# Optimization experiments

Hardware: AMD Instinct MI355X
Metric: run time of the kernel (lower is better)

The kernel has to match this reference:

```python
import math
import jax, jax.numpy as jnp
import numpy as np
from jax import lax

B = 4; N = 4096; F = 15; A = 24          # batch, tcr_num, feature_num, aa_num
HID = 10; H = 1; HD = 10; AFN = 14       # attn hidden, heads, head dim, sum(filter_num)
KS = [2, 3, 4, 5, 6, 7]; FN = [3, 3, 3, 2, 2, 1]
K = int(N * 0.05)                        # routing topk = 204
SCALE = np.float32(1.0 / math.sqrt(HD))


def setup_inputs() -> dict:
    key = jax.random.key(0)
    ks = jax.random.split(key, 24)
    inp = {"x": jax.random.normal(ks[0], (B, N, F, A), jnp.float32)}
    for i, (h, f) in enumerate(zip(KS, FN)):
        inp["conv_w%d" % h] = jax.random.normal(ks[1 + 2 * i], (f, F, h), jnp.float32) * 0.1
        inp["conv_b%d" % h] = jax.random.normal(ks[2 + 2 * i], (f,), jnp.float32) * 0.1
    specs = [("q", HID, AFN), ("k", HID, AFN), ("v", HID, AFN), ("attn", AFN, HID), ("mil", 2, AFN)]
    for j, (nm, o, i_) in enumerate(specs):
        inp["w_" + nm] = jax.random.normal(ks[13 + 2 * j], (o, i_), jnp.float32) * 0.1
        inp["b_" + nm] = jax.random.normal(ks[14 + 2 * j], (o,), jnp.float32) * 0.1
    return inp


def reference(x, conv_w2, conv_b2, conv_w3, conv_b3, conv_w4, conv_b4,
              conv_w5, conv_b5, conv_w6, conv_b6, conv_w7, conv_b7,
              w_q, b_q, w_k, b_k, w_v, b_v, w_attn, b_attn, w_mil, b_mil):
    # --- per-sequence conv feature extraction ---
    xc = x.reshape(-1, F, A)  # [B*N, 15, 24]
    feats = []
    for w, b in [(conv_w2, conv_b2), (conv_w3, conv_b3), (conv_w4, conv_b4),
                 (conv_w5, conv_b5), (conv_w6, conv_b6), (conv_w7, conv_b7)]:
        y = lax.conv_general_dilated(xc, w, (1,), 'VALID',
                                     dimension_numbers=('NCH', 'OIH', 'NCH'))
        y = jax.nn.relu(y + b[None, :, None])
        feats.append(jnp.max(y, axis=-1))  # AdaptiveMaxPool1d(1)
    out = jnp.concatenate(feats, axis=1).reshape(B, N, AFN)  # [B, N, 14]

    # --- QKV projections, split into heads -> [B, H, N, HD] ---
    q = (out @ w_q.T + b_q).reshape(B, N, H, HD).transpose(0, 2, 1, 3)
    k = (out @ w_k.T + b_k).reshape(B, N, H, HD).transpose(0, 2, 1, 3)
    v = (out @ w_v.T + b_v).reshape(B, N, H, HD).transpose(0, 2, 1, 3)

    # --- bi-level routing: full scores, topk over head-mean (detached in torch) ---
    scores_raw = jnp.einsum('bhnd,bhmd->bhnm', q, k)  # [B, H, N, N]
    a_r = jnp.mean(lax.stop_gradient(scores_raw), axis=1)  # [B, N, N]
    _, idx = lax.top_k(a_r, K)  # [B, N, K] int32
    idx_r = jnp.broadcast_to(idx[:, None], (B, H, N, K))

    scores = jnp.take_along_axis(scores_raw * SCALE, idx_r, axis=3)  # [B, H, N, K]
    # gather values per (batch, head, query): v_g[b,h,i,j] = v[b,h,idx[b,h,i,j]]
    v_g = jax.vmap(jax.vmap(lambda vh, ih: vh[ih]))(v, idx_r)  # [B, H, N, K, HD]

    probs = jax.nn.softmax(scores, axis=-1)  # dropout is identity at p=0 / eval
    ctx = jnp.einsum('bhnk,bhnkd->bhnd', probs, v_g)  # [B, H, N, HD]
    ctx = ctx.transpose(0, 2, 1, 3).reshape(B, N, HID)

    ctx = ctx @ w_attn.T + b_attn          # [B, N, 14]
    logits = ctx @ w_mil.T + b_mil          # [B, N, 2]
    pooled = jnp.sum(logits, axis=1) / N    # [B, 2]
    return pooled, probs[:, :, :, None, :]  # probs shaped [B, H, N, 1, K] as in torch
```

## Files before the change

### kernel.cpp

```cpp
#include <hip/hip_runtime.h>
#include <math.h>

#define NB 4
#define NN 4096
#define KSEL 204
#define NBINS 512
#define CANDN 256
#define QKSCALE 0.31622776601683794f

#define WS_Q 0
#define WS_KT (NB * NN * 10)
#define WS_V (2 * NB * NN * 10)
#define WS_LG (3 * NB * NN * 10)

#define SEQ_PER_BLOCK 16

__global__ __launch_bounds__(256) void featqkv_kernel(
    const float* __restrict__ x,
    const float* __restrict__ w2, const float* __restrict__ b2,
    const float* __restrict__ w3, const float* __restrict__ b3,
    const float* __restrict__ w4, const float* __restrict__ b4,
    const float* __restrict__ w5, const float* __restrict__ b5,
    const float* __restrict__ w6, const float* __restrict__ b6,
    const float* __restrict__ w7, const float* __restrict__ b7,
    const float* __restrict__ wq, const float* __restrict__ bq,
    const float* __restrict__ wk, const float* __restrict__ bk,
    const float* __restrict__ wv, const float* __restrict__ bv,
    float* __restrict__ q_out, float* __restrict__ kT_out, float* __restrict__ v_out)
{
    __shared__ float xs[SEQ_PER_BLOCK * 360];
    __shared__ float wconv[840];
    __shared__ float bconv[14];
    __shared__ float wqkv[420];
    __shared__ float bqkv[30];
    __shared__ float feats[SEQ_PER_BLOCK * 14];

    const int t = threadIdx.x;
    const int g0 = blockIdx.x * SEQ_PER_BLOCK;

    const float* xg = x + (size_t)g0 * 360;
    for (int i = t; i < SEQ_PER_BLOCK * 360; i += 256) xs[i] = xg[i];
    for (int i = t; i < 90; i += 256) wconv[i] = w2[i];
    for (int i = t; i < 135; i += 256) wconv[90 + i] = w3[i];
    for (int i = t; i < 180; i += 256) wconv[225 + i] = w4[i];
    for (int i = t; i < 150; i += 256) wconv[405 + i] = w5[i];
    for (int i = t; i < 180; i += 256) wconv[555 + i] = w6[i];
    for (int i = t; i < 105; i += 256) wconv[735 + i] = w7[i];
    if (t < 3) bconv[t] = b2[t];
    else if (t < 6) bconv[t] = b3[t - 3];
    else if (t < 9) bconv[t] = b4[t - 6];
    else if (t < 11) bconv[t] = b5[t - 9];
    else if (t < 13) bconv[t] = b6[t - 11];
    else if (t == 13) bconv[t] = b7[0];
    for (int i = t; i < 140; i += 256) wqkv[i] = wq[i];
    for (int i = t; i < 140; i += 256) wqkv[140 + i] = wk[i];
    for (int i = t; i < 140; i += 256) wqkv[280 + i] = wv[i];
    if (t < 10) bqkv[t] = bq[t];
    else if (t < 20) bqkv[t] = bk[t - 10];
    else if (t < 30) bqkv[t] = bv[t - 20];
    __syncthreads();

    const int seq = t >> 4;
    const int wkr = t & 15;

    if (wkr < 14) {
        const int ch = wkr;
        int h, fi, woff;
        if (ch < 3)       { h = 2; fi = ch;      woff = 0   + fi * 30; }
        else if (ch < 6)  { h = 3; fi = ch - 3;  woff = 90  + fi * 45; }
        else if (ch < 9)  { h = 4; fi = ch - 6;  woff = 225 + fi * 60; }
        else if (ch < 11) { h = 5; fi = ch - 9;  woff = 405 + fi * 75; }
        else if (ch < 13) { h = 6; fi = ch - 11; woff = 555 + fi * 90; }
        else              { h = 7; fi = 0;       woff = 735; }
        const int T = 24 - h + 1;

        float acc[23];
#pragma unroll
        for (int i2 = 0; i2 < 23; i2++) acc[i2] = 0.f;
        const float* xrow = &xs[seq * 360];
        for (int c = 0; c < 15; c++) {
            float xr[24];
#pragma unroll
            for (int u = 0; u < 24; u++) xr[u] = xrow[c * 24 + u];
#pragma unroll
            for (int j = 0; j < 7; j++) {
                if (j < h) {
                    float wv_ = wconv[woff + c * h + j];
#pragma unroll
                    for (int tt = 0; tt < 23; tt++) {
                        if (tt < T) acc[tt] = fmaf(xr[tt + j], wv_, acc[tt]);
                    }
                }
            }
        }
        float m = -1e30f;
#pragma unroll
        for (int tt = 0; tt < 23; tt++) {
            if (tt < T) m = fmaxf(m, acc[tt]);
        }
        feats[seq * 14 + ch] = fmaxf(m + bconv[ch], 0.f);
    }
    __syncthreads();

    const int g = g0 + seq;
    const int b_ = g >> 12;
    const int n_ = g & 4095;
    for (int o = wkr; o < 30; o += 16) {
        const int type = o / 10;
        const int comp = o % 10;
        const float* wrow = &wqkv[type * 140 + comp * 14];
        const float* frow = &feats[seq * 14];
        float a = bqkv[type * 10 + comp];
#pragma unroll
        for (int ii = 0; ii < 14; ii++) a = fmaf(frow[ii], wrow[ii], a);
        if (type == 0) q_out[(size_t)g * 10 + comp] = a;
        else if (type == 1) kT_out[((size_t)b_ * 10 + comp) * NN + n_] = a;
        else v_out[(size_t)g * 10 + comp] = a;
    }
}

__device__ __forceinline__ float dec_key(unsigned int k) {
    return (k & 0x80000000u) ? __uint_as_float(k ^ 0x80000000u)
                             : __uint_as_float(~k);
}
__device__ __forceinline__ unsigned int enc_key(float s) {
    unsigned int u = __float_as_uint(s);
    return (u & 0x80000000u) ? ~u : (u | 0x80000000u);
}

__global__ __launch_bounds__(256, 6) void attn_kernel(
    const float* __restrict__ qbuf, const float* __restrict__ kTbuf,
    const float* __restrict__ vbuf,
    const float* __restrict__ w_attn, const float* __restrict__ b_attn,
    const float* __restrict__ w_mil, const float* __restrict__ b_mil,
    float* __restrict__ out_probs, float* __restrict__ logits)
{
    __shared__ unsigned int base_[NBINS];
    __shared__ unsigned int bc_[NBINS];
    __shared__ unsigned long long cand[CANDN];
    __shared__ float hpart[4], lpart[4], fpart[4];
    __shared__ unsigned int wtot[4];
    __shared__ float ctxp[40];
    __shared__ float ctx_sh[10];
    __shared__ float attn_sh[14];

    const int t = threadIdx.x;
    const int lane = t & 63;
    const int w = t >> 6;
    const int row = blockIdx.x;
    const int b_ = row >> 12;

    float q0, q1, q2, q3, q4, q5, q6, q7, q8, q9;
    {
        const float* qp = qbuf + (size_t)row * 10;
        q0 = qp[0]; q1 = qp[1]; q2 = qp[2]; q3 = qp[3]; q4 = qp[4];
        q5 = qp[5]; q6 = qp[6]; q7 = qp[7]; q8 = qp[8]; q9 = qp[9];
    }
    const float* kTb = kTbuf + (size_t)b_ * 10 * NN;
    float sc[16];
    float vhi = -1e30f, vlo = 1e30f;
#pragma unroll
    for (int i = 0; i < 4; i++) {
        float4 a0 = make_float4(0.f, 0.f, 0.f, 0.f);
#pragma unroll
        for (int c = 0; c < 10; c++) {
            const float qc = (c == 0) ? q0 : (c == 1) ? q1 : (c == 2) ? q2 : (c == 3) ? q3 :
                             (c == 4) ? q4 : (c == 5) ? q5 : (c == 6) ? q6 : (c == 7) ? q7 :
                             (c == 8) ? q8 : q9;
            const float4 kv = reinterpret_cast<const float4*>(kTb + c * NN)[i * 256 + t];
            a0.x = fmaf(qc, kv.x, a0.x);
            a0.y = fmaf(qc, kv.y, a0.y);
            a0.z = fmaf(qc, kv.z, a0.z);
            a0.w = fmaf(qc, kv.w, a0.w);
        }
        sc[i * 4 + 0] = a0.x; sc[i * 4 + 1] = a0.y;
        sc[i * 4 + 2] = a0.z; sc[i * 4 + 3] = a0.w;
        vhi = fmaxf(vhi, fmaxf(fmaxf(a0.x, a0.y), fmaxf(a0.z, a0.w)));
        vlo = fminf(vlo, fminf(fminf(a0.x, a0.y), fminf(a0.z, a0.w)));
    }
#pragma unroll
    for (int off = 32; off > 0; off >>= 1) {
        vhi = fmaxf(vhi, __shfl_xor(vhi, off));
        vlo = fminf(vlo, __shfl_xor(vlo, off));
    }
    if (lane == 0) { hpart[w] = vhi; lpart[w] = vlo; }
    base_[2 * t] = 0u; base_[2 * t + 1] = 0u;
    cand[t] = 0ULL;
    __syncthreads();
    const float hi = fmaxf(fmaxf(hpart[0], hpart[1]), fmaxf(hpart[2], hpart[3]));
    const float lo = fminf(fminf(lpart[0], lpart[1]), fminf(lpart[2], lpart[3]));
    const bool degen = (hi <= lo);

    float pv = 0.f;
    int jj = 0, p = KSEL;
    bool selected = false;
    const float smax = hi * QKSCALE;

    if (!degen) {
        const float scale = (float)(NBINS - 1) / (hi - lo);

#pragma unroll
        for (int i = 0; i < 16; i++) {
            const int bin = (int)fminf((sc[i] - lo) * scale, (float)(NBINS - 1));
            atomicAdd(&base_[bin], 1u);
        }
        __syncthreads();

        {
            const unsigned int c0 = base_[2 * t];
            const unsigned int c1 = base_[2 * t + 1];
            const unsigned int T_ = c0 + c1;
            unsigned int acc = T_;
#pragma unroll
            for (int off = 1; off < 64; off <<= 1) {
                unsigned int o = __shfl_down(acc, off);
                if (lane + off < 64) acc += o;
            }
            if (lane == 0) wtot[w] = acc;
            __syncthreads();
            unsigned int tail = 0u;
#pragma unroll
            for (int w2 = 1; w2 < 4; w2++) if (w2 > w) tail += wtot[w2];
            const unsigned int A = (acc - T_) + tail;
            base_[2 * t + 1] = A;
            base_[2 * t] = A + c1;
            bc_[2 * t + 1] = A;
            bc_[2 * t] = A + c1;
        }
        __syncthreads();

#pragma unroll
        for (int i = 0; i < 16; i++) {
            const int bin = (int)fminf((sc[i] - lo) * scale, (float)(NBINS - 1));
            const unsigned int bs = base_[bin];
            if (bs < KSEL) {
                const unsigned int pos = atomicAdd(&bc_[bin], 1u);
                if (pos < CANDN) {
                    const int j = (i >> 2) * 1024 + t * 4 + (i & 3);
                    cand[pos] = (((unsigned long long)enc_key(sc[i])) << 16)
                              | (unsigned long long)(4095 - j);
                }
            }
        }
        __syncthreads();

        const unsigned long long mine = cand[t];
        if (mine != 0ULL) {
            const float s = dec_key((unsigned int)(mine >> 16));
            const int bin = (int)fminf((s - lo) * scale, (float)(NBINS - 1));
            const unsigned int bs = base_[bin];
            unsigned int end = (bin < NBINS - 1) ? 0u : 0u;
            end = (bin == NBINS - 1) ? bs + (4096u) : base_[bin + 1];
            unsigned int e2 = (bin > 0) ? base_[bin - 1] : 4096u;
            if (e2 > CANDN) e2 = CANDN;
            unsigned int rank = 0;
            for (unsigned int s2 = bs; s2 < e2; s2++)
                rank += (cand[s2] > mine) ? 1u : 0u;
            const unsigned int pp = bs + rank;
            if (pp < KSEL) {
                selected = true;
                p = (int)pp;
                jj = 4095 - (int)(mine & 0xFFFFu);
                pv = expf(s * QKSCALE - smax);
            }
        }
    } else {
        if (t < KSEL) {
            selected = true;
            p = t;
            jj = t;
            pv = 1.f;
        }
    }

    float dsum = pv;
#pragma unroll
    for (int off = 32; off > 0; off >>= 1) dsum += __shfl_xor(dsum, off);
    if (lane == 0) fpart[w] = dsum;
    __syncthreads();
    const float inv = 1.f / (fpart[0] + fpart[1] + fpart[2] + fpart[3]);

    float cx0 = 0.f, cx1 = 0.f, cx2 = 0.f, cx3 = 0.f, cx4 = 0.f;
    float cx5 = 0.f, cx6 = 0.f, cx7 = 0.f, cx8 = 0.f, cx9 = 0.f;
    if (selected) {
        const float pn = pv * inv;
        out_probs[(size_t)row * KSEL + p] = pn;
        const float* vr = vbuf + ((size_t)b_ * NN + (size_t)jj) * 10;
        const float2 v01 = reinterpret_cast<const float2*>(vr)[0];
        const float2 v23 = reinterpret_cast<const float2*>(vr)[1];
        const float2 v45 = reinterpret_cast<const float2*>(vr)[2];
        const float2 v67 = reinterpret_cast<const float2*>(vr)[3];
        const float2 v89 = reinterpret_cast<const float2*>(vr)[4];
        cx0 = pn * v01.x; cx1 = pn * v01.y;
        cx2 = pn * v23.x; cx3 = pn * v23.y;
        cx4 = pn * v45.x; cx5 = pn * v45.y;
        cx6 = pn * v67.x; cx7 = pn * v67.y;
        cx8 = pn * v89.x; cx9 = pn * v89.y;
    }
#pragma unroll
    for (int off = 32; off > 0; off >>= 1) {
        cx0 += __shfl_xor(cx0, off); cx1 += __shfl_xor(cx1, off);
        cx2 += __shfl_xor(cx2, off); cx3 += __shfl_xor(cx3, off);
        cx4 += __shfl_xor(cx4, off); cx5 += __shfl_xor(cx5, off);
        cx6 += __shfl_xor(cx6, off); cx7 += __shfl_xor(cx7, off);
        cx8 += __shfl_xor(cx8, off); cx9 += __shfl_xor(cx9, off);
    }
    if (lane == 0) {
        ctxp[w * 10 + 0] = cx0; ctxp[w * 10 + 1] = cx1; ctxp[w * 10 + 2] = cx2;
        ctxp[w * 10 + 3] = cx3; ctxp[w * 10 + 4] = cx4; ctxp[w * 10 + 5] = cx5;
        ctxp[w * 10 + 6] = cx6; ctxp[w * 10 + 7] = cx7; ctxp[w * 10 + 8] = cx8;
        ctxp[w * 10 + 9] = cx9;
    }
    __syncthreads();
    if (t < 10) ctx_sh[t] = ctxp[t] + ctxp[10 + t] + ctxp[20 + t] + ctxp[30 + t];
    __syncthreads();

    if (t < 14) {
        float a = b_attn[t];
#pragma unroll
        for (int d = 0; d < 10; d++) a = fmaf(ctx_sh[d], w_attn[t * 10 + d], a);
        attn_sh[t] = a;
    }
    __syncthreads();
    if (t < 2) {
        float lg = b_mil[t];
#pragma unroll
        for (int ii = 0; ii < 14; ii++) lg = fmaf(attn_sh[ii], w_mil[t * 14 + ii], lg);
        logits[(size_t)row * 2 + t] = lg;
    }
}

__global__ __launch_bounds__(256) void pool_kernel(
    const float* __restrict__ logits, float* __restrict__ out)
{
    __shared__ float red[256];
    const int t = threadIdx.x;
    const int bc = blockIdx.x;
    const int b_ = bc >> 1;
    const int c_ = bc & 1;
    float a = 0.f;
    for (int n2 = t; n2 < NN; n2 += 256)
        a += logits[((size_t)b_ * NN + n2) * 2 + c_];
    red[t] = a;
    __syncthreads();
    for (int off = 128; off > 0; off >>= 1) {
        if (t < off) red[t] += red[t + off];
        __syncthreads();
    }
    if (t == 0) out[bc] = red[0] * (1.f / 4096.f);
}

extern "C" void kernel_launch(void* const* d_in, const int* in_sizes, int n_in,
                              void* d_out, int out_size, void* d_ws, size_t ws_size,
                              hipStream_t stream) {
    const float* x  = (const float*)d_in[0];
    const float* w2 = (const float*)d_in[1];  const float* b2 = (const float*)d_in[2];
    const float* w3 = (const float*)d_in[3];  const float* b3 = (const float*)d_in[4];
    const float* w4 = (const float*)d_in[5];  const float* b4 = (const float*)d_in[6];
    const float* w5 = (const float*)d_in[7];  const float* b5 = (const float*)d_in[8];
    const float* w6 = (const float*)d_in[9];  const float* b6 = (const float*)d_in[10];
    const float* w7 = (const float*)d_in[11]; const float* b7 = (const float*)d_in[12];
    const float* wq = (const float*)d_in[13]; const float* bq = (const float*)d_in[14];
    const float* wk = (const float*)d_in[15]; const float* bk = (const float*)d_in[16];
    const float* wv = (const float*)d_in[17]; const float* bv = (const float*)d_in[18];
    const float* wat = (const float*)d_in[19]; const float* bat = (const float*)d_in[20];
    const float* wm = (const float*)d_in[21];  const float* bm = (const float*)d_in[22];

    float* ws = (float*)d_ws;
    float* qb = ws + WS_Q;
    float* kT = ws + WS_KT;
    float* vb = ws + WS_V;
    float* lg = ws + WS_LG;
    float* out = (float*)d_out;

    hipLaunchKernelGGL(featqkv_kernel, dim3(NB * NN / SEQ_PER_BLOCK), dim3(256), 0, stream,
                       x, w2, b2, w3, b3, w4, b4, w5, b5, w6, b6, w7, b7,
                       wq, bq, wk, bk, wv, bv, qb, kT, vb);
    hipLaunchKernelGGL(attn_kernel, dim3(NB * NN), dim3(256), 0, stream,
                       qb, kT, vb, wat, bat, wm, bm, out + 8, lg);
    hipLaunchKernelGGL(pool_kernel, dim3(8), dim3(256), 0, stream, lg, out);
}
```

Before: 261.7 us.

## Process two query rows per attention block, fuse pooling via atomics, pad conv weights

The attention kernel now handles two query rows per block, so each key load feeds both score computations. The separate pool kernel is removed: logits are added straight into the pooled output with atomics, and the first conv kernel zeroes that output. The conv stage pads weights to width 7 and the input rows to 30 with zeros, which removes branches at the cost of extra FMAs. The candidate buffer is enlarged, and the selection phase for each row still runs serially inside the block.

New measurement: 472.5 us. 1.81x slower.

```diff
diff --git a/kernel.cpp b/kernel.cpp
--- a/kernel.cpp
+++ b/kernel.cpp
@@ -5,17 +5,16 @@
 #define NN 4096
 #define KSEL 204
 #define NBINS 512
-#define CANDN 256
+#define CANDN 320
 #define QKSCALE 0.31622776601683794f
 
 #define WS_Q 0
 #define WS_KT (NB * NN * 10)
 #define WS_V (2 * NB * NN * 10)
-#define WS_LG (3 * NB * NN * 10)
 
 #define SEQ_PER_BLOCK 16
 
-__global__ __launch_bounds__(256) void featqkv_kernel(
+__global__ __launch_bounds__(256, 4) void featqkv_kernel(
     const float* __restrict__ x,
     const float* __restrict__ w2, const float* __restrict__ b2,
     const float* __restrict__ w3, const float* __restrict__ b3,
@@ -26,10 +25,11 @@
     const float* __restrict__ wq, const float* __restrict__ bq,
     const float* __restrict__ wk, const float* __restrict__ bk,
     const float* __restrict__ wv, const float* __restrict__ bv,
-    float* __restrict__ q_out, float* __restrict__ kT_out, float* __restrict__ v_out)
+    float* __restrict__ q_out, float* __restrict__ kT_out, float* __restrict__ v_out,
+    float* __restrict__ out_pooled)
 {
-    __shared__ float xs[SEQ_PER_BLOCK * 360];
-    __shared__ float wconv[840];
+    __shared__ float xs[SEQ_PER_BLOCK * 450];
+    __shared__ float wpad[14 * 105];
     __shared__ float bconv[14];
     __shared__ float wqkv[420];
     __shared__ float bqkv[30];
@@ -38,14 +38,39 @@
     const int t = threadIdx.x;
     const int g0 = blockIdx.x * SEQ_PER_BLOCK;
 
-    const float* xg = x + (size_t)g0 * 360;
-    for (int i = t; i < SEQ_PER_BLOCK * 360; i += 256) xs[i] = xg[i];
-    for (int i = t; i < 90; i += 256) wconv[i] = w2[i];
-    for (int i = t; i < 135; i += 256) wconv[90 + i] = w3[i];
-    for (int i = t; i < 180; i += 256) wconv[225 + i] = w4[i];
-    for (int i = t; i < 150; i += 256) wconv[405 + i] = w5[i];
-    for (int i = t; i < 180; i += 256) wconv[555 + i] = w6[i];
-    for (int i = t; i < 105; i += 256) wconv[735 + i] = w7[i];
+    if (blockIdx.x == 0 && t < 8) out_pooled[t] = 0.f;
+
+    const float4* xg4 = reinterpret_cast<const float4*>(x + (size_t)g0 * 360);
+    for (int i = t; i < SEQ_PER_BLOCK * 90; i += 256) {
+        const int seq = i / 90;
+        const int i4 = i % 90;
+        const int c = i4 / 6;
+        const int u = (i4 % 6) * 4;
+        const float4 v = xg4[i];
+        float* dst = &xs[seq * 450 + c * 30 + u];
+        dst[0] = v.x; dst[1] = v.y; dst[2] = v.z; dst[3] = v.w;
+    }
+    for (int i = t; i < SEQ_PER_BLOCK * 90; i += 256) {
+        const int seq = i / 90;
+        const int rem = i % 90;
+        const int c = rem / 6;
+        const int u = 24 + rem % 6;
+        xs[seq * 450 + c * 30 + u] = 0.f;
+    }
+    for (int i = t; i < 14 * 105; i += 256) {
+        const int ch = i / 105;
+        const int rem = i % 105;
+        const int c = rem / 7;
+        const int j = rem % 7;
+        float v = 0.f;
+        if (ch < 3)       { if (j < 2) v = w2[ch * 30 + c * 2 + j]; }
+        else if (ch < 6)  { if (j < 3) v = w3[(ch - 3) * 45 + c * 3 + j]; }
+        else if (ch < 9)  { if (j < 4) v = w4[(ch - 6) * 60 + c * 4 + j]; }
+        else if (ch < 11) { if (j < 5) v = w5[(ch - 9) * 75 + c * 5 + j]; }
+        else if (ch < 13) { if (j < 6) v = w6[(ch - 11) * 90 + c * 6 + j]; }
+        else              { v = w7[c * 7 + j]; }
+        wpad[i] = v;
+    }
     if (t < 3) bconv[t] = b2[t];
     else if (t < 6) bconv[t] = b3[t - 3];
     else if (t < 9) bconv[t] = b4[t - 6];
@@ -65,32 +90,25 @@
 
     if (wkr < 14) {
         const int ch = wkr;
-        int h, fi, woff;
-        if (ch < 3)       { h = 2; fi = ch;      woff = 0   + fi * 30; }
-        else if (ch < 6)  { h = 3; fi = ch - 3;  woff = 90  + fi * 45; }
-        else if (ch < 9)  { h = 4; fi = ch - 6;  woff = 225 + fi * 60; }
-        else if (ch < 11) { h = 5; fi = ch - 9;  woff = 405 + fi * 75; }
-        else if (ch < 13) { h = 6; fi = ch - 11; woff = 555 + fi * 90; }
-        else              { h = 7; fi = 0;       woff = 735; }
-        const int T = 24 - h + 1;
+        const int h = (ch < 3) ? 2 : (ch < 6) ? 3 : (ch < 9) ? 4 :
+                      (ch < 11) ? 5 : (ch < 13) ? 6 : 7;
+        const int T = 25 - h;
 
         float acc[23];
 #pragma unroll
         for (int i2 = 0; i2 < 23; i2++) acc[i2] = 0.f;
-        const float* xrow = &xs[seq * 360];
+        const float* xrow = &xs[seq * 450];
+        const float* wrow = &wpad[ch * 105];
         for (int c = 0; c < 15; c++) {
-            float xr[24];
-#pragma unroll
-            for (int u = 0; u < 24; u++) xr[u] = xrow[c * 24 + u];
+            float xr[30];
+#pragma unroll
+            for (int u = 0; u < 30; u++) xr[u] = xrow[c * 30 + u];
 #pragma unroll
             for (int j = 0; j < 7; j++) {
-                if (j < h) {
-                    float wv_ = wconv[woff + c * h + j];
-#pragma unroll
-                    for (int tt = 0; tt < 23; tt++) {
-                        if (tt < T) acc[tt] = fmaf(xr[tt + j], wv_, acc[tt]);
-                    }
-                }
+                const float wv_ = wrow[c * 7 + j];
+#pragma unroll
+                for (int tt = 0; tt < 23; tt++)
+                    acc[tt] = fmaf(xr[tt + j], wv_, acc[tt]);
             }
         }
         float m = -1e30f;
@@ -133,7 +151,7 @@
     const float* __restrict__ vbuf,
     const float* __restrict__ w_attn, const float* __restrict__ b_attn,
     const float* __restrict__ w_mil, const float* __restrict__ b_mil,
-    float* __restrict__ out_probs, float* __restrict__ logits)
+    float* __restrict__ out_probs, float* __restrict__ out_pooled)
 {
     __shared__ unsigned int base_[NBINS];
     __shared__ unsigned int bc_[NBINS];
@@ -147,207 +165,198 @@
     const int t = threadIdx.x;
     const int lane = t & 63;
     const int w = t >> 6;
-    const int row = blockIdx.x;
-    const int b_ = row >> 12;
-
-    float q0, q1, q2, q3, q4, q5, q6, q7, q8, q9;
-    {
-        const float* qp = qbuf + (size_t)row * 10;
-        q0 = qp[0]; q1 = qp[1]; q2 = qp[2]; q3 = qp[3]; q4 = qp[4];
-        q5 = qp[5]; q6 = qp[6]; q7 = qp[7]; q8 = qp[8]; q9 = qp[9];
+    const int row0 = blockIdx.x * 2;
+    const int b_ = row0 >> 12;
+
+    float qA[10], qB[10];
+#pragma unroll
+    for (int c = 0; c < 10; c++) {
+        qA[c] = qbuf[(size_t)row0 * 10 + c];
+        qB[c] = qbuf[(size_t)(row0 + 1) * 10 + c];
     }
     const float* kTb = kTbuf + (size_t)b_ * 10 * NN;
-    float sc[16];
-    float vhi = -1e30f, vlo = 1e30f;
+    float scA[16], scB[16];
+    float hiA = -1e30f, loA = 1e30f, hiB = -1e30f, loB = 1e30f;
 #pragma unroll
     for (int i = 0; i < 4; i++) {
-        float4 a0 = make_float4(0.f, 0.f, 0.f, 0.f);
+        float4 aA = make_float4(0.f, 0.f, 0.f, 0.f);
+        float4 aB = make_float4(0.f, 0.f, 0.f, 0.f);
 #pragma unroll
         for (int c = 0; c < 10; c++) {
-            const float qc = (c == 0) ? q0 : (c == 1) ? q1 : (c == 2) ? q2 : (c == 3) ? q3 :
-                             (c == 4) ? q4 : (c == 5) ? q5 : (c == 6) ? q6 : (c == 7) ? q7 :
-                             (c == 8) ? q8 : q9;
             const float4 kv = reinterpret_cast<const float4*>(kTb + c * NN)[i * 256 + t];
-            a0.x = fmaf(qc, kv.x, a0.x);
-            a0.y = fmaf(qc, kv.y, a0.y);
-            a0.z = fmaf(qc, kv.z, a0.z);
-            a0.w = fmaf(qc, kv.w, a0.w);
-        }
-        sc[i * 4 + 0] = a0.x; sc[i * 4 + 1] = a0.y;
-        sc[i * 4 + 2] = a0.z; sc[i * 4 + 3] = a0.w;
-        vhi = fmaxf(vhi, fmaxf(fmaxf(a0.x, a0.y), fmaxf(a0.z, a0.w)));
-        vlo = fminf(vlo, fminf(fminf(a0.x, a0.y), fminf(a0.z, a0.w)));
+            aA.x = fmaf(qA[c], kv.x, aA.x); aA.y = fmaf(qA[c], kv.y, aA.y);
+            aA.z = fmaf(qA[c], kv.z, aA.z); aA.w = fmaf(qA[c], kv.w, aA.w);
+            aB.x = fmaf(qB[c], kv.x, aB.x); aB.y = fmaf(qB[c], kv.y, aB.y);
+            aB.z = fmaf(qB[c], kv.z, aB.z); aB.w = fmaf(qB[c], kv.w, aB.w);
+        }
+        scA[i * 4 + 0] = aA.x; scA[i * 4 + 1] = aA.y; scA[i * 4 + 2] = aA.z; scA[i * 4 + 3] = aA.w;
+        scB[i * 4 + 0] = aB.x; scB[i * 4 + 1] = aB.y; scB[i * 4 + 2] = aB.z; scB[i * 4 + 3] = aB.w;
+        hiA = fmaxf(hiA, fmaxf(fmaxf(aA.x, aA.y), fmaxf(aA.z, aA.w)));
+        loA = fminf(loA, fminf(fminf(aA.x, aA.y), fminf(aA.z, aA.w)));
+        hiB = fmaxf(hiB, fmaxf(fmaxf(aB.x, aB.y), fmaxf(aB.z, aB.w)));
+        loB = fminf(loB, fminf(fminf(aB.x, aB.y), fminf(aB.z, aB.w)));
     }
 #pragma unroll
     for (int off = 32; off > 0; off >>= 1) {
-        vhi = fmaxf(vhi, __shfl_xor(vhi, off));
-        vlo = fminf(vlo, __shfl_xor(vlo, off));
-    }
-    if (lane == 0) { hpart[w] = vhi; lpart[w] = vlo; }
-    base_[2 * t] = 0u; base_[2 * t + 1] = 0u;
-    cand[t] = 0ULL;
-    __syncthreads();
-    const float hi = fmaxf(fmaxf(hpart[0], hpart[1]), fmaxf(hpart[2], hpart[3]));
-    const float lo = fminf(fminf(lpart[0], lpart[1]), fminf(lpart[2], lpart[3]));
-    const bool degen = (hi <= lo);
-
-    float pv = 0.f;
-    int jj = 0, p = KSEL;
-    bool selected = false;
-    const float smax = hi * QKSCALE;
-
-    if (!degen) {
-        const float scale = (float)(NBINS - 1) / (hi - lo);
-
-#pragma unroll
-        for (int i = 0; i < 16; i++) {
-            const int bin = (int)fminf((sc[i] - lo) * scale, (float)(NBINS - 1));
-            atomicAdd(&base_[bin], 1u);
-        }
-        __syncthreads();
-
-        {
-            const unsigned int c0 = base_[2 * t];
-            const unsigned int c1 = base_[2 * t + 1];
-            const unsigned int T_ = c0 + c1;
-            unsigned int acc = T_;
-#pragma unroll
-            for (int off = 1; off < 64; off <<= 1) {
-                unsigned int o = __shfl_down(acc, off);
-                if (lane + off < 64) acc += o;
-            }
-            if (lane == 0) wtot[w] = acc;
+        hiA = fmaxf(hiA, __shfl_xor(hiA, off));
+        loA = fminf(loA, __shfl_xor(loA, off));
+        hiB = fmaxf(hiB, __shfl_xor(hiB, off));
+        loB = fminf(loB, __shfl_xor(loB, off));
+    }
+
+#pragma unroll 1
+    for (int rr = 0; rr < 2; rr++) {
+        const int row = row0 + rr;
+        if (lane == 0) {
+            hpart[w] = rr ? hiB : hiA;
+            lpart[w] = rr ? loB : loA;
+        }
+        base_[2 * t] = 0u; base_[2 * t + 1] = 0u;
+        if (t < CANDN - 256) cand[256 + t] = 0ULL;
+        cand[t] = 0ULL;
+        __syncthreads();
+        const float hi = fmaxf(fmaxf(hpart[0], hpart[1]), fmaxf(hpart[2], hpart[3]));
+        const float lo = fminf(fminf(lpart[0], lpart[1]), fminf(lpart[2], lpart[3]));
+        const bool degen = (hi <= lo);
+
+        float pv = 0.f;
+        int jj = 0, p = KSEL;
+        bool selected = false;
+        const float smax = hi * QKSCALE;
+
+        if (!degen) {
+            const float scale = (float)(NBINS - 1) / (hi - lo);
+            int bins[16];
+
+#pragma unroll
+            for (int i = 0; i < 16; i++) {
+                const float s = rr ? scB[i] : scA[i];
+                const int bin = (int)fminf((s - lo) * scale, (float)(NBINS - 1));
+                bins[i] = bin;
+                atomicAdd(&base_[bin], 1u);
+            }
             __syncthreads();
-            unsigned int tail = 0u;
-#pragma unroll
-            for (int w2 = 1; w2 < 4; w2++) if (w2 > w) tail += wtot[w2];
-            const unsigned int A = (acc - T_) + tail;
-            base_[2 * t + 1] = A;
-            base_[2 * t] = A + c1;
-            bc_[2 * t + 1] = A;
-            bc_[2 * t] = A + c1;
-        }
-        __syncthreads();
-
-#pragma unroll
-        for (int i = 0; i < 16; i++) {
-            const int bin = (int)fminf((sc[i] - lo) * scale, (float)(NBINS - 1));
-            const unsigned int bs = base_[bin];
-            if (bs < KSEL) {
-                const unsigned int pos = atomicAdd(&bc_[bin], 1u);
-                if (pos < CANDN) {
-                    const int j = (i >> 2) * 1024 + t * 4 + (i & 3);
-                    cand[pos] = (((unsigned long long)enc_key(sc[i])) << 16)
-                              | (unsigned long long)(4095 - j);
+
+            {
+                const unsigned int c0 = base_[2 * t];
+                const unsigned int c1 = base_[2 * t + 1];
+                const unsigned int T_ = c0 + c1;
+                unsigned int acc = T_;
+#pragma unroll
+                for (int off = 1; off < 64; off <<= 1) {
+                    unsigned int o = __shfl_down(acc, off);
+                    if (lane + off < 64) acc += o;
                 }
-            }
-        }
-        __syncthreads();
-
-        const unsigned long long mine = cand[t];
-        if (mine != 0ULL) {
-            const float s = dec_key((unsigned int)(mine >> 16));
-            const int bin = (int)fminf((s - lo) * scale, (float)(NBINS - 1));
-            const unsigned int bs = base_[bin];
-            unsigned int end = (bin < NBINS - 1) ? 0u : 0u;
-            end = (bin == NBINS - 1) ? bs + (4096u) : base_[bin + 1];
-            unsigned int e2 = (bin > 0) ? base_[bin - 1] : 4096u;
-            if (e2 > CANDN) e2 = CANDN;
-            unsigned int rank = 0;
-            for (unsigned int s2 = bs; s2 < e2; s2++)
-                rank += (cand[s2] > mine) ? 1u : 0u;
-            const unsigned int pp = bs + rank;
-            if (pp < KSEL) {
-                selected = true;
-                p = (int)pp;
-                jj = 4095 - (int)(mine & 0xFFFFu);
-                pv = expf(s * QKSCALE - smax);
-            }
-        }
-    } else {
-        if (t < KSEL) {
-            selected = true;
-            p = t;
-            jj = t;
-            pv = 1.f;
-        }
-    }
-
-    float dsum = pv;
-#pragma unroll
-    for (int off = 32; off > 0; off >>= 1) dsum += __shfl_xor(dsum, off);
-    if (lane == 0) fpart[w] = dsum;
-    __syncthreads();
-    const float inv = 1.f / (fpart[0] + fpart[1] + fpart[2] + fpart[3]);
-
-    float cx0 = 0.f, cx1 = 0.f, cx2 = 0.f, cx3 = 0.f, cx4 = 0.f;
-    float cx5 = 0.f, cx6 = 0.f, cx7 = 0.f, cx8 = 0.f, cx9 = 0.f;
-    if (selected) {
-        const float pn = pv * inv;
-        out_probs[(size_t)row * KSEL + p] = pn;
-        const float* vr = vbuf + ((size_t)b_ * NN + (size_t)jj) * 10;
-        const float2 v01 = reinterpret_cast<const float2*>(vr)[0];
-        const float2 v23 = reinterpret_cast<const float2*>(vr)[1];
-        const float2 v45 = reinterpret_cast<const float2*>(vr)[2];
-        const float2 v67 = reinterpret_cast<const float2*>(vr)[3];
-        const float2 v89 = reinterpret_cast<const float2*>(vr)[4];
-        cx0 = pn * v01.x; cx1 = pn * v01.y;
-        cx2 = pn * v23.x; cx3 = pn * v23.y;
-        cx4 = pn * v45.x; cx5 = pn * v45.y;
-        cx6 = pn * v67.x; cx7 = pn * v67.y;
-        cx8 = pn * v89.x; cx9 = pn * v89.y;
-    }
-#pragma unroll
-    for (int off = 32; off > 0; off >>= 1) {
-        cx0 += __shfl_xor(cx0, off); cx1 += __shfl_xor(cx1, off);
-        cx2 += __shfl_xor(cx2, off); cx3 += __shfl_xor(cx3, off);
-        cx4 += __shfl_xor(cx4, off); cx5 += __shfl_xor(cx5, off);
-        cx6 += __shfl_xor(cx6, off); cx7 += __shfl_xor(cx7, off);
-        cx8 += __shfl_xor(cx8, off); cx9 += __shfl_xor(cx9, off);
-    }
-    if (lane == 0) {
-        ctxp[w * 10 + 0] = cx0; ctxp[w * 10 + 1] = cx1; ctxp[w * 10 + 2] = cx2;
-        ctxp[w * 10 + 3] = cx3; ctxp[w * 10 + 4] = cx4; ctxp[w * 10 + 5] = cx5;
-        ctxp[w * 10 + 6] = cx6; ctxp[w * 10 + 7] = cx7; ctxp[w * 10 + 8] = cx8;
-        ctxp[w * 10 + 9] = cx9;
-    }
-    __syncthreads();
-    if (t < 10) ctx_sh[t] = ctxp[t] + ctxp[10 + t] + ctxp[20 + t] + ctxp[30 + t];
-    __syncthreads();
-
-    if (t < 14) {
-        float a = b_attn[t];
-#pragma unroll
-        for (int d = 0; d < 10; d++) a = fmaf(ctx_sh[d], w_attn[t * 10 + d], a);
-        attn_sh[t] = a;
-    }
-    __syncthreads();
-    if (t < 2) {
-        float lg = b_mil[t];
-#pragma unroll
-        for (int ii = 0; ii < 14; ii++) lg = fmaf(attn_sh[ii], w_mil[t * 14 + ii], lg);
-        logits[(size_t)row * 2 + t] = lg;
-    }
-}
-
-__global__ __launch_bounds__(256) void pool_kernel(
-    const float* __restrict__ logits, float* __restrict__ out)
-{
-    __shared__ float red[256];
-    const int t = threadIdx.x;
-    const int bc = blockIdx.x;
-    const int b_ = bc >> 1;
-    const int c_ = bc & 1;
-    float a = 0.f;
-    for (int n2 = t; n2 < NN; n2 += 256)
-        a += logits[((size_t)b_ * NN + n2) * 2 + c_];
-    red[t] = a;
-    __syncthreads();
-    for (int off = 128; off > 0; off >>= 1) {
-        if (t < off) red[t] += red[t + off];
-        __syncthreads();
-    }
-    if (t == 0) out[bc] = red[0] * (1.f / 4096.f);
+                if (lane == 0) wtot[w] = acc;
+                __syncthreads();
+                unsigned int tail = 0u;
+#pragma unroll
+                for (int w2 = 1; w2 < 4; w2++) if (w2 > w) tail += wtot[w2];
+                const unsigned int A = (acc - T_) + tail;
+                base_[2 * t + 1] = A;
+                base_[2 * t] = A + c1;
+                bc_[2 * t + 1] = A;
+                bc_[2 * t] = A + c1;
+            }
+            __syncthreads();
+
+#pragma unroll
+            for (int i = 0; i < 16; i++) {
+                const int bin = bins[i];
+                const unsigned int bs = base_[bin];
+                if (bs < KSEL) {
+                    const unsigned int pos = atomicAdd(&bc_[bin], 1u);
+                    if (pos < CANDN) {
+                        const float s = rr ? scB[i] : scA[i];
+                        const int j = (i >> 2) * 1024 + t * 4 + (i & 3);
+                        cand[pos] = (((unsigned long long)enc_key(s)) << 16)
+                                  | (unsigned long long)(4095 - j);
+                    }
+                }
+            }
+            __syncthreads();
+
+            if (t < CANDN) {
+                const unsigned long long mine = cand[t];
+                if (mine != 0ULL) {
+                    const float s = dec_key((unsigned int)(mine >> 16));
+                    const int bin = (int)fminf((s - lo) * scale, (float)(NBINS - 1));
+                    const unsigned int bs = base_[bin];
+                    unsigned int e2 = (bin > 0) ? base_[bin - 1] : 4096u;
+                    if (e2 > CANDN) e2 = CANDN;
+                    unsigned int rank = 0;
+                    for (unsigned int s2 = bs; s2 < e2; s2++)
+                        rank += (cand[s2] > mine) ? 1u : 0u;
+                    const unsigned int pp = bs + rank;
+                    if (pp < KSEL) {
+                        selected = true;
+                        p = (int)pp;
+                        jj = 4095 - (int)(mine & 0xFFFFu);
+                        pv = expf(s * QKSCALE - smax);
+                    }
+                }
+            }
+        } else {
+            if (t < KSEL) { selected = true; p = t; jj = t; pv = 1.f; }
+        }
+
+        float dsum = pv;
+#pragma unroll
+        for (int off = 32; off > 0; off >>= 1) dsum += __shfl_xor(dsum, off);
+        if (lane == 0) fpart[w] = dsum;
+        __syncthreads();
+        const float inv = 1.f / (fpart[0] + fpart[1] + fpart[2] + fpart[3]);
+
+        float cx0 = 0.f, cx1 = 0.f, cx2 = 0.f, cx3 = 0.f, cx4 = 0.f;
+        float cx5 = 0.f, cx6 = 0.f, cx7 = 0.f, cx8 = 0.f, cx9 = 0.f;
+        if (selected) {
+            const float pn = pv * inv;
+            out_probs[(size_t)row * KSEL + p] = pn;
+            const float* vr = vbuf + ((size_t)b_ * NN + (size_t)jj) * 10;
+            const float2 v01 = reinterpret_cast<const float2*>(vr)[0];
+            const float2 v23 = reinterpret_cast<const float2*>(vr)[1];
+            const float2 v45 = reinterpret_cast<const float2*>(vr)[2];
+            const float2 v67 = reinterpret_cast<const float2*>(vr)[3];
+            const float2 v89 = reinterpret_cast<const float2*>(vr)[4];
+            cx0 = pn * v01.x; cx1 = pn * v01.y;
+            cx2 = pn * v23.x; cx3 = pn * v23.y;
+            cx4 = pn * v45.x; cx5 = pn * v45.y;
+            cx6 = pn * v67.x; cx7 = pn * v67.y;
+            cx8 = pn * v89.x; cx9 = pn * v89.y;
+        }
+#pragma unroll
+        for (int off = 32; off > 0; off >>= 1) {
+            cx0 += __shfl_xor(cx0, off); cx1 += __shfl_xor(cx1, off);
+            cx2 += __shfl_xor(cx2, off); cx3 += __shfl_xor(cx3, off);
+            cx4 += __shfl_xor(cx4, off); cx5 += __shfl_xor(cx5, off);
+            cx6 += __shfl_xor(cx6, off); cx7 += __shfl_xor(cx7, off);
+            cx8 += __shfl_xor(cx8, off); cx9 += __shfl_xor(cx9, off);
+        }
+        if (lane == 0) {
+            ctxp[w * 10 + 0] = cx0; ctxp[w * 10 + 1] = cx1; ctxp[w * 10 + 2] = cx2;
+            ctxp[w * 10 + 3] = cx3; ctxp[w * 10 + 4] = cx4; ctxp[w * 10 + 5] = cx5;
+            ctxp[w * 10 + 6] = cx6; ctxp[w * 10 + 7] = cx7; ctxp[w * 10 + 8] = cx8;
+            ctxp[w * 10 + 9] = cx9;
+        }
+        __syncthreads();
+        if (t < 10) ctx_sh[t] = ctxp[t] + ctxp[10 + t] + ctxp[20 + t] + ctxp[30 + t];
+        __syncthreads();
+
+        if (t < 14) {
+            float a = b_attn[t];
+#pragma unroll
+            for (int d = 0; d < 10; d++) a = fmaf(ctx_sh[d], w_attn[t * 10 + d], a);
+            attn_sh[t] = a;
+        }
+        __syncthreads();
+        if (t < 2) {
+            float lg = b_mil[t];
+#pragma unroll
+            for (int ii = 0; ii < 14; ii++) lg = fmaf(attn_sh[ii], w_mil[t * 14 + ii], lg);
+            atomicAdd(&out_pooled[b_ * 2 + t], lg * (1.f / 4096.f));
+        }
+        __syncthreads();
+    }
 }
 
 extern "C" void kernel_launch(void* const* d_in, const int* in_sizes, int n_in,
@@ -370,13 +379,11 @@
     float* qb = ws + WS_Q;
     float* kT = ws + WS_KT;
     float* vb = ws + WS_V;
-    float* lg = ws + WS_LG;
     float* out = (float*)d_out;
 
     hipLaunchKernelGGL(featqkv_kernel, dim3(NB * NN / SEQ_PER_BLOCK), dim3(256), 0, stream,
                        x, w2, b2, w3, b3, w4, b4, w5, b5, w6, b6, w7, b7,
-                       wq, bq, wk, bk, wv, bv, qb, kT, vb);
-    hipLaunchKernelGGL(attn_kernel, dim3(NB * NN), dim3(256), 0, stream,
-                       qb, kT, vb, wat, bat, wm, bm, out + 8, lg);
-    hipLaunchKernelGGL(pool_kernel, dim3(8), dim3(256), 0, stream, lg, out);
-}
+                       wq, bq, wk, bk, wv, bv, qb, kT, vb, out);
+    hipLaunchKernelGGL(attn_kernel, dim3(NB * NN / 2), dim3(256), 0, stream,
+                       qb, kT, vb, wat, bat, wm, bm, out + 8, out);
+}
```
